# Kernel optimization log

Measured on AMD Instinct MI355X. Metric: run time of the kernel, lower is better.

## Reference

```python
import jax, jax.numpy as jnp
import numpy as np

DT = 0.01  # discretization step


def _discretize(log_omega, zeta_logit, P, Q, B):
    """Bilinear (Tustin) discretization of DPLR A = diag(lambda) + P Q^T."""
    omega = jnp.exp(log_omega)
    zeta = jax.nn.sigmoid(zeta_logit)
    real = -zeta * omega
    imag = omega * jnp.sqrt(jnp.clip(1.0 - zeta * zeta, 1e-8, None))
    lam = jax.lax.complex(real, imag)                      # (n,) complex eigenvalues
    A = jnp.diag(lam) + (P @ Q.T).astype(lam.dtype)        # (n, n) complex
    n = A.shape[0]
    I = jnp.eye(n, dtype=A.dtype)
    I_minus = I - (DT / 2.0) * A
    I_plus = I + (DT / 2.0) * A
    A_d = jnp.linalg.solve(I_minus, I_plus)                # (n, n)
    B_d = jnp.linalg.solve(I_minus, B.astype(A.dtype) * jnp.sqrt(jnp.float32(DT)))  # (n, d_in)
    return A_d, B_d


def setup_inputs() -> dict:
    key = jax.random.key(0)
    ks = jax.random.split(key, 8)
    n, r, d_in, d_out = 64, 4, 128, 128
    batch, seq = 32, 8192
    log_omega = jax.random.uniform(ks[0], (n,)) * (np.log(0.1) - np.log(0.01)) + np.log(0.01)
    return {
        "u": jax.random.normal(ks[1], (batch, seq, d_in), dtype=jnp.float32),
        "log_omega": log_omega.astype(jnp.float32),
        "zeta_logit": (jax.random.normal(ks[2], (n,)) * 0.5).astype(jnp.float32),
        "P": (jax.random.normal(ks[3], (n, r)) * 0.1).astype(jnp.float32),
        "Q": (jax.random.normal(ks[4], (n, r)) * 0.1).astype(jnp.float32),
        "B": (jax.random.normal(ks[5], (n, d_in)) * 0.1).astype(jnp.float32),
        "C": (jax.random.normal(ks[6], (d_out, n)) * 0.1).astype(jnp.float32),
        "D": jnp.zeros((d_out, d_in), dtype=jnp.float32),
    }


def reference(u, log_omega, zeta_logit, P, Q, B, C, D):
    A_d, B_d = _discretize(log_omega, zeta_logit, P, Q, B)
    cdt = A_d.dtype
    uc = u.astype(cdt)                                     # (b, t, d_in)
    # Precompute input injections and feedthrough as batched GEMMs.
    bu = jnp.einsum('bti,ni->btn', uc, B_d)                # (b, t, n)
    du = jnp.einsum('bti,oi->bto', uc, D.astype(cdt))      # (b, t, d_out)

    def step(x, bu_t):                                     # x: (b, n)
        x = x @ A_d.T + bu_t
        return x, x

    x0 = jnp.zeros((u.shape[0], A_d.shape[0]), dtype=cdt)
    _, xs = jax.lax.scan(step, x0, jnp.swapaxes(bu, 0, 1))  # (t, b, n)
    xs = jnp.swapaxes(xs, 0, 1)                             # (b, t, n)
    y = jnp.einsum('btn,on->bto', xs, C.astype(cdt)) + du
    return y.real
```

## Files before the change

### kernel.cpp

```cpp
#include <hip/hip_runtime.h>

#define OFF_E      0L
#define OFF_E2     8192L
#define OFF_AD     16384L
#define OFF_P0     24576L
#define OFF_P1     32768L
#define OFF_AHAT   40960L
#define OFF_ALHAT  57344L
#define OFF_WBU    73728L
#define OFF_EST    90112L
#define OFF_SIN    614400L
#define OFF_XR     1138688L
#define OFF_FW1H   8192L
#define OFF_FW1L   16384L
#define OFF_FCH    24576L
#define OFF_FCL    28672L
#define OFF_FDH    32768L
#define OFF_FDL    40960L

typedef __attribute__((ext_vector_type(8))) short short8;
typedef __attribute__((ext_vector_type(4))) float f32x4;

union U4S8 { uint4 u; short8 s; };
union S8U  { ushort h[8]; short8 s; };


__global__ void build_E(const float* __restrict__ lw, const float* __restrict__ zl,
                        const float* __restrict__ P, const float* __restrict__ Q,
                        float2* __restrict__ E)
{
    int idx = blockIdx.x * 256 + threadIdx.x;
    if (idx >= 4096) return;
    int i = idx >> 6, j = idx & 63;
    float pq = 0.f;
    #pragma unroll
    for (int r = 0; r < 4; ++r) pq += P[i*4+r] * Q[j*4+r];
    float ex = pq, ey = 0.f;
    if (i == j) {
        float om = expf(lw[i]);
        float ze = 1.f / (1.f + expf(-zl[i]));
        ex += -ze * om;
        ey  = om * sqrtf(fmaxf(1.f - ze*ze, 1e-8f));
    }
    E[idx] = make_float2(0.005f * ex, 0.005f * ey);
}

__global__ __launch_bounds__(256) void cgemm64(const float2* __restrict__ A,
                                               const float2* __restrict__ B,
                                               float2* __restrict__ Co,
                                               int aI, int bI, int post)
{
    int g = blockIdx.x * 256 + threadIdx.x;
    #pragma unroll
    for (int q = 0; q < 4; ++q) {
        int idx = g + q * 1024;
        int i = idx >> 6, j = idx & 63;
        float accx = 0.f, accy = 0.f;
        for (int k = 0; k < 64; ++k) {
            float2 a = A[i*64 + k];
            if (aI && k == i) a.x += 1.f;
            float2 b = B[k*64 + j];
            if (bI && k == j) b.x += 1.f;
            accx += a.x*b.x - a.y*b.y;
            accy += a.x*b.y + a.y*b.x;
        }
        if (post) { accx = 2.f*accx - (i == j ? 1.f : 0.f); accy = 2.f*accy; }
        Co[idx] = make_float2(accx, accy);
    }
}

__global__ __launch_bounds__(256) void k_bd(const float2* __restrict__ Ad,
                                            const float* __restrict__ Bm,
                                            float* __restrict__ Wbu)
{
    int idx = blockIdx.x * 256 + threadIdx.x;
    int n = idx >> 7, i = idx & 127;
    float ar = 0.f, ai = 0.f;
    for (int m = 0; m < 64; ++m) {
        float2 a = Ad[n*64 + m];
        float b = Bm[m*128 + i];
        ar += a.x * b; ai += a.y * b;
    }
    ar += Bm[n*128 + i];
    Wbu[n*128 + i]      = 0.05f * ar;
    Wbu[(64+n)*128 + i] = 0.05f * ai;
}

__global__ void k_embed(const float2* __restrict__ Ad, const float2* __restrict__ M64,
                        float* __restrict__ Ahat, float* __restrict__ ALhat)
{
    int idx = blockIdx.x * 256 + threadIdx.x;
    int sel = idx >> 14;
    int rem = idx & 16383;
    int i = rem >> 7, j = rem & 127;
    const float2* S = sel ? M64 : Ad;
    float2 v = S[(i & 63)*64 + (j & 63)];
    float o = (i < 64) ? ((j < 64) ? v.x : -v.y)
                       : ((j < 64) ? v.y :  v.x);
    (sel ? ALhat : Ahat)[i*128 + j] = o;
}

__global__ void k_swz(const float* __restrict__ Ahat, ushort* __restrict__ DTf)
{
    int t = blockIdx.x * 256 + threadIdx.x;
    if (t >= 2048) return;
    int lane = t & 63, kt = (t >> 6) & 3, nt = t >> 8;
    int n = (lane & 15) + nt * 16;
    int kbase = (lane >> 4) * 8 + kt * 32;
    #pragma unroll
    for (int j = 0; j < 8; ++j) {
        int k = kbase + j;
        float d = Ahat[n * 128 + k] - (n == k ? 1.f : 0.f);
        uint u = __float_as_uint(d);
        DTf[t * 8 + j] = (ushort)((u + 0x7FFFu + ((u >> 16) & 1)) >> 16);
    }
}

__device__ __forceinline__ ushort rne_bf16(float v) {
    uint u = __float_as_uint(v);
    return (ushort)((u + 0x7FFFu + ((u >> 16) & 1u)) >> 16);
}

__global__ void k_wfrag(const float* __restrict__ W, int KT,
                        ushort* __restrict__ FHi, ushort* __restrict__ FLo)
{
    int total = 8 * KT * 64;
    int t = blockIdx.x * 256 + threadIdx.x;
    if (t >= total) return;
    int K = KT * 32;
    int lane = t & 63;
    int kt = (t >> 6) % KT;
    int nt = t / (64 * KT);
    int n = (lane & 15) + nt * 16;
    int kbase = (lane >> 4) * 8 + kt * 32;
    #pragma unroll
    for (int j = 0; j < 8; ++j) {
        float v = W[n * K + kbase + j];
        ushort h = rne_bf16(v);
        float vh = __uint_as_float(((uint)h) << 16);
        ushort lo = rne_bf16(v - vh);
        FHi[t * 8 + j] = h;
        FLo[t * 8 + j] = lo;
    }
}

__device__ __forceinline__ void split8(const float* __restrict__ xf, short8& hi, short8& lo) {
    S8U H, L;
    #pragma unroll
    for (int j = 0; j < 8; ++j) {
        float v = xf[j];
        uint u = __float_as_uint(v);
        uint hbits = (u + 0x7FFFu + ((u >> 16) & 1u)) & 0xFFFF0000u;
        H.h[j] = (ushort)(hbits >> 16);
        float r = v - __uint_as_float(hbits);
        uint ur = __float_as_uint(r);
        L.h[j] = (ushort)((ur + 0x7FFFu + ((ur >> 16) & 1u)) >> 16);
    }
    hi = H.s; lo = L.s;
}

template<int KT1, int KT2>
__global__ __launch_bounds__(256) void gemm_mfma(
    const float* __restrict__ X1, const uint4* __restrict__ F1h, const uint4* __restrict__ F1l,
    const float* __restrict__ X2, const uint4* __restrict__ F2h, const uint4* __restrict__ F2l,
    float* __restrict__ Y)
{
    constexpr int KT2P = (KT2 > 0) ? KT2 : 1;
    int l = threadIdx.x & 63, w = threadIdx.x >> 6;
    int m = l & 15, q = l >> 4;

    short8 f1h[2][KT1], f1l[2][KT1];
    #pragma unroll
    for (int nt = 0; nt < 2; ++nt)
        #pragma unroll
        for (int kt = 0; kt < KT1; ++kt) {
            int f = ((w*2 + nt)*KT1 + kt)*64 + l;
            U4S8 a; a.u = F1h[f]; f1h[nt][kt] = a.s;
            U4S8 b; b.u = F1l[f]; f1l[nt][kt] = b.s;
        }
    short8 f2h[2][KT2P], f2l[2][KT2P];
    if constexpr (KT2 > 0) {
        #pragma unroll
        for (int nt = 0; nt < 2; ++nt)
            #pragma unroll
            for (int kt = 0; kt < KT2; ++kt) {
                int f = ((w*2 + nt)*KT2 + kt)*64 + l;
                U4S8 a; a.u = F2h[f]; f2h[nt][kt] = a.s;
                U4S8 b; b.u = F2l[f]; f2l[nt][kt] = b.s;
            }
    }

    long row0 = (long)blockIdx.x * 64;
    const float* x1p = X1 + (row0 + m) * (KT1*32) + q*8;
    const float* x2p = (KT2 > 0) ? (X2 + (row0 + m) * (KT2P*32) + q*8) : nullptr;
    float* yp = Y + (row0 + q*4) * 128 + w*32 + m;

    float4 xa[KT1 + KT2P][2], xb[KT1 + KT2P][2];

    auto loadt = [&](float4 (&dst)[KT1 + KT2P][2], int rt) {
        long o1 = (long)rt * 16 * (KT1*32);
        #pragma unroll
        for (int kt = 0; kt < KT1; ++kt) {
            const float* p = x1p + o1 + kt*32;
            dst[kt][0] = *(const float4*)p;
            dst[kt][1] = *(const float4*)(p + 4);
        }
        if constexpr (KT2 > 0) {
            long o2 = (long)rt * 16 * (KT2*32);
            #pragma unroll
            for (int kt = 0; kt < KT2; ++kt) {
                const float* p = x2p + o2 + kt*32;
                dst[KT1 + kt][0] = *(const float4*)p;
                dst[KT1 + kt][1] = *(const float4*)(p + 4);
            }
        }
    };

    auto compute = [&](float4 (&xr)[KT1 + KT2P][2], int rt) {
        f32x4 acc[2];
        acc[0] = (f32x4){0.f, 0.f, 0.f, 0.f};
        acc[1] = (f32x4){0.f, 0.f, 0.f, 0.f};
        #pragma unroll
        for (int kt = 0; kt < KT1; ++kt) {
            short8 ah, al;
            split8((const float*)&xr[kt][0], ah, al);
            #pragma unroll
            for (int nt = 0; nt < 2; ++nt) {
                acc[nt] = __builtin_amdgcn_mfma_f32_16x16x32_bf16(ah, f1h[nt][kt], acc[nt], 0, 0, 0);
                acc[nt] = __builtin_amdgcn_mfma_f32_16x16x32_bf16(al, f1h[nt][kt], acc[nt], 0, 0, 0);
                acc[nt] = __builtin_amdgcn_mfma_f32_16x16x32_bf16(ah, f1l[nt][kt], acc[nt], 0, 0, 0);
            }
        }
        if constexpr (KT2 > 0) {
            #pragma unroll
            for (int kt = 0; kt < KT2; ++kt) {
                short8 ah, al;
                split8((const float*)&xr[KT1 + kt][0], ah, al);
                #pragma unroll
                for (int nt = 0; nt < 2; ++nt) {
                    acc[nt] = __builtin_amdgcn_mfma_f32_16x16x32_bf16(ah, f2h[nt][kt], acc[nt], 0, 0, 0);
                    acc[nt] = __builtin_amdgcn_mfma_f32_16x16x32_bf16(al, f2h[nt][kt], acc[nt], 0, 0, 0);
                    acc[nt] = __builtin_amdgcn_mfma_f32_16x16x32_bf16(ah, f2l[nt][kt], acc[nt], 0, 0, 0);
                }
            }
        }
        #pragma unroll
        for (int nt = 0; nt < 2; ++nt)
            #pragma unroll
            for (int r = 0; r < 4; ++r)
                yp[(long)rt*16*128 + r*128 + nt*16] = acc[nt][r];
    };

    loadt(xa, 0);
    loadt(xb, 1);
    compute(xa, 0);
    loadt(xa, 2);
    compute(xb, 1);
    loadt(xb, 3);
    compute(xa, 2);
    compute(xb, 3);
}

template <int PASS>
__global__ __launch_bounds__(64, 1) void mfma_scan(
    const uint4* __restrict__ DTf, const float* __restrict__ bu,
    const float* __restrict__ sIn, float* __restrict__ eOut,
    float* __restrict__ xrOut)
{
    __shared__ ushort xlds[16 * 136];
    int l    = threadIdx.x;
    int col  = l & 15;
    int quad = l >> 4;
    int wid  = blockIdx.x;

    short8 dtf[8][4];
    #pragma unroll
    for (int nt = 0; nt < 8; ++nt)
        #pragma unroll
        for (int kt = 0; kt < 4; ++kt) {
            U4S8 u; u.u = DTf[(nt*4 + kt)*64 + l];
            dtf[nt][kt] = u.s;
        }

    int  rowg0 = wid * 16;
    long b  = rowg0 >> 7;
    long c0 = rowg0 & 127;

    f32x4 acc[8];
    #pragma unroll
    for (int nt = 0; nt < 8; ++nt) acc[nt] = (f32x4){0.f, 0.f, 0.f, 0.f};
    if constexpr (PASS == 3) {
        #pragma unroll
        for (int nt = 0; nt < 8; ++nt)
            #pragma unroll
            for (int r = 0; r < 4; ++r)
                acc[nt][r] = sIn[(long)(rowg0 + quad*4 + r)*128 + col + nt*16];
    }

    long buBase[4], xrBase[4];
    #pragma unroll
    for (int r = 0; r < 4; ++r) {
        int m = quad*4 + r;
        long tbase = b*8192 + (c0 + m)*64;
        buBase[r] = tbase*128 + col;
        xrBase[r] = tbase*64 + col;
    }

    float buA[8][4], buB[8][4];
    #define LOADBU(dst, TAU) { long _t = (TAU); _Pragma("unroll") \
        for (int nt = 0; nt < 8; ++nt) { _Pragma("unroll") \
            for (int r = 0; r < 4; ++r) dst[nt][r] = bu[buBase[r] + _t*128 + nt*16]; } }

    auto dostep = [&](float (&bucur)[8][4], int TAU) {
        asm volatile("" ::: "memory");
        #pragma unroll
        for (int nt = 0; nt < 8; ++nt)
            #pragma unroll
            for (int r = 0; r < 4; ++r) {
                uint u = __float_as_uint(acc[nt][r]);
                xlds[(quad*4 + r)*136 + col + nt*16] = (ushort)((u + 0x8000u) >> 16);
            }
        asm volatile("" ::: "memory");
        short8 af[4];
        #pragma unroll
        for (int kt = 0; kt < 4; ++kt) {
            U4S8 u; u.u = *(const uint4*)&xlds[col*136 + quad*8 + kt*32];
            af[kt] = u.s;
        }
        #pragma unroll
        for (int nt = 0; nt < 8; ++nt)
            #pragma unroll
            for (int r = 0; r < 4; ++r) acc[nt][r] += bucur[nt][r];
        #pragma unroll
        for (int kt = 0; kt < 4; ++kt)
            #pragma unroll
            for (int nt = 0; nt < 8; ++nt)
                acc[nt] = __builtin_amdgcn_mfma_f32_16x16x32_bf16(af[kt], dtf[nt][kt], acc[nt], 0, 0, 0);
        if constexpr (PASS == 3) {
            #pragma unroll
            for (int nt = 0; nt < 4; ++nt)
                #pragma unroll
                for (int r = 0; r < 4; ++r)
                    xrOut[xrBase[r] + (long)TAU*64 + nt*16] = acc[nt][r];
        }
    };

    LOADBU(buA, 0);
    for (int tau = 0; tau < 64; tau += 2) {
        LOADBU(buB, tau + 1);
        dostep(buA, tau);
        LOADBU(buA, (tau + 2 < 64) ? (tau + 2) : 63);
        dostep(buB, tau + 1);
    }

    if constexpr (PASS == 1) {
        #pragma unroll
        for (int nt = 0; nt < 8; ++nt)
            #pragma unroll
            for (int r = 0; r < 4; ++r)
                eOut[(long)(rowg0 + quad*4 + r)*128 + col + nt*16] = acc[nt][r];
    }
    #undef LOADBU
}

template <int PH>
__global__ __launch_bounds__(64, 1) void phase2k(
    const uint4* __restrict__ Bh, const uint4* __restrict__ Bl,
    const float* __restrict__ eIn, const float* __restrict__ seedIn,
    float* __restrict__ outPtr)
{
    constexpr int NSTEP = (PH == 2) ? 8 : 16;
    __shared__ ushort xh[16 * 136];
    __shared__ ushort xl[16 * 136];
    int l = threadIdx.x;
    int col = l & 15, quad = l >> 4;
    int wid = blockIdx.x;

    short8 bh[8][4], bl[8][4];
    #pragma unroll
    for (int nt = 0; nt < 8; ++nt)
        #pragma unroll
        for (int kt = 0; kt < 4; ++kt) {
            U4S8 a; a.u = Bh[(nt*4 + kt)*64 + l]; bh[nt][kt] = a.s;
            U4S8 b; b.u = Bl[(nt*4 + kt)*64 + l]; bl[nt][kt] = b.s;
        }

    long eBase[4], oBase[4];
    #pragma unroll
    for (int r = 0; r < 4; ++r) {
        int g = wid*16 + quad*4 + r;
        if constexpr (PH == 2) {
            eBase[r] = (long)g * 1024;
            oBase[r] = (long)g * 1024;
        } else {
            int b = g >> 3, seg = g & 7;
            eBase[r] = ((long)b*128 + seg*16) * 128;
            oBase[r] = (PH == 1) ? (long)g * 128 : eBase[r];
        }
    }

    f32x4 acc[8];
    #pragma unroll
    for (int nt = 0; nt < 8; ++nt) acc[nt] = (f32x4){0.f, 0.f, 0.f, 0.f};
    if constexpr (PH == 3) {
        #pragma unroll
        for (int nt = 0; nt < 8; ++nt)
            #pragma unroll
            for (int r = 0; r < 4; ++r)
                acc[nt][r] = seedIn[(long)(wid*16 + quad*4 + r)*128 + col + nt*16];
    }

    float eA[8][4], eB[8][4];
    #define LOADE(dst, C) { long _c = (C); _Pragma("unroll") \
        for (int nt = 0; nt < 8; ++nt) { _Pragma("unroll") \
            for (int r = 0; r < 4; ++r) dst[nt][r] = eIn[eBase[r] + _c*128 + col + nt*16]; } }

    auto dostep = [&](float (&ecur)[8][4], int c) {
        if constexpr (PH >= 2) {
            #pragma unroll
            for (int nt = 0; nt < 8; ++nt)
                #pragma unroll
                for (int r = 0; r < 4; ++r)
                    outPtr[oBase[r] + (long)c*128 + col + nt*16] = acc[nt][r];
        }
        asm volatile("" ::: "memory");
        #pragma unroll
        for (int nt = 0; nt < 8; ++nt)
            #pragma unroll
            for (int r = 0; r < 4; ++r) {
                float v = acc[nt][r];
                uint u = __float_as_uint(v);
                int off = (quad*4 + r)*136 + col + nt*16;
                xh[off] = (ushort)(u >> 16);
                float rr = v - __uint_as_float(u & 0xFFFF0000u);
                xl[off] = (ushort)(__float_as_uint(rr) >> 16);
            }
        asm volatile("" ::: "memory");
        short8 ah[4], al[4];
        #pragma unroll
        for (int kt = 0; kt < 4; ++kt) {
            U4S8 u1; u1.u = *(const uint4*)&xh[col*136 + quad*8 + kt*32]; ah[kt] = u1.s;
            U4S8 u2; u2.u = *(const uint4*)&xl[col*136 + quad*8 + kt*32]; al[kt] = u2.s;
        }
        #pragma unroll
        for (int nt = 0; nt < 8; ++nt)
            #pragma unroll
            for (int r = 0; r < 4; ++r) acc[nt][r] = ecur[nt][r];
        #pragma unroll
        for (int kt = 0; kt < 4; ++kt)
            #pragma unroll
            for (int nt = 0; nt < 8; ++nt)
                acc[nt] = __builtin_amdgcn_mfma_f32_16x16x32_bf16(ah[kt], bh[nt][kt], acc[nt], 0, 0, 0);
        #pragma unroll
        for (int kt = 0; kt < 4; ++kt)
            #pragma unroll
            for (int nt = 0; nt < 8; ++nt)
                acc[nt] = __builtin_amdgcn_mfma_f32_16x16x32_bf16(al[kt], bh[nt][kt], acc[nt], 0, 0, 0);
        #pragma unroll
        for (int kt = 0; kt < 4; ++kt)
            #pragma unroll
            for (int nt = 0; nt < 8; ++nt)
                acc[nt] = __builtin_amdgcn_mfma_f32_16x16x32_bf16(ah[kt], bl[nt][kt], acc[nt], 0, 0, 0);
    };

    LOADE(eA, 0);
    for (int c = 0; c < NSTEP; c += 2) {
        LOADE(eB, c + 1);
        dostep(eA, c);
        LOADE(eA, (c + 2 < NSTEP) ? (c + 2) : (NSTEP - 1));
        dostep(eB, c + 1);
    }

    if constexpr (PH == 1) {
        #pragma unroll
        for (int nt = 0; nt < 8; ++nt)
            #pragma unroll
            for (int r = 0; r < 4; ++r)
                outPtr[oBase[r] + col + nt*16] = acc[nt][r];
    }
    #undef LOADE
}


extern "C" void kernel_launch(void* const* d_in, const int* in_sizes, int n_in,
                              void* d_out, int out_size, void* d_ws, size_t ws_size,
                              hipStream_t stream) {
    const float* u  = (const float*)d_in[0];
    const float* lw = (const float*)d_in[1];
    const float* zl = (const float*)d_in[2];
    const float* P  = (const float*)d_in[3];
    const float* Q  = (const float*)d_in[4];
    const float* Bm = (const float*)d_in[5];
    const float* Cm = (const float*)d_in[6];
    const float* Dm = (const float*)d_in[7];
    float* y = (float*)d_out;
    float* w = (float*)d_ws;

    float2* E   = (float2*)(w + OFF_E);
    float2* E2  = (float2*)(w + OFF_E2);
    float2* AD  = (float2*)(w + OFF_AD);
    float2* P0  = (float2*)(w + OFF_P0);
    float2* P1  = (float2*)(w + OFF_P1);
    float*  Ahat  = w + OFF_AHAT;
    float*  ALhat = w + OFF_ALHAT;
    float*  Wbu   = w + OFF_WBU;
    float*  Est   = w + OFF_EST;
    float*  SIn   = w + OFF_SIN;
    float*  XR    = w + OFF_XR;
    ushort* DTf   = (ushort*)(w + OFF_E);
    ushort* FW1H  = (ushort*)(w + OFF_FW1H);
    ushort* FW1L  = (ushort*)(w + OFF_FW1L);
    ushort* FCH   = (ushort*)(w + OFF_FCH);
    ushort* FCL   = (ushort*)(w + OFF_FCL);
    ushort* FDH   = (ushort*)(w + OFF_FDH);
    ushort* FDL   = (ushort*)(w + OFF_FDL);
    float*  E2s   = w + OFF_XR;
    float*  S2s   = w + OFF_XR + 32768L;
    ushort* ALHH  = (ushort*)(w + OFF_XR + 65536L);
    ushort* ALHL  = (ushort*)(w + OFF_XR + 73728L);
    ushort* M16H  = (ushort*)(w + OFF_XR + 81920L);
    ushort* M16L  = (ushort*)(w + OFF_XR + 90112L);

    build_E<<<16, 256, 0, stream>>>(lw, zl, P, Q, E);
    cgemm64<<<4, 256, 0, stream>>>(E, E, E2, 0, 0, 0);
    cgemm64<<<4, 256, 0, stream>>>(E, E2, AD, 1, 1, 1);
    k_bd<<<32, 256, 0, stream>>>(AD, Bm, Wbu);
    cgemm64<<<4, 256, 0, stream>>>(AD, AD, P0, 0, 0, 0);
    cgemm64<<<4, 256, 0, stream>>>(P0, P0, P1, 0, 0, 0);
    cgemm64<<<4, 256, 0, stream>>>(P1, P1, P0, 0, 0, 0);
    cgemm64<<<4, 256, 0, stream>>>(P0, P0, P1, 0, 0, 0);
    cgemm64<<<4, 256, 0, stream>>>(P1, P1, P0, 0, 0, 0);
    cgemm64<<<4, 256, 0, stream>>>(P0, P0, P1, 0, 0, 0);
    k_embed<<<128, 256, 0, stream>>>(AD, P1, Ahat, ALhat);
    k_swz<<<8, 256, 0, stream>>>(Ahat, DTf);
    k_wfrag<<<8, 256, 0, stream>>>(ALhat, 4, ALHH, ALHL);
    cgemm64<<<4, 256, 0, stream>>>(P1, P1, P0, 0, 0, 0);
    cgemm64<<<4, 256, 0, stream>>>(P0, P0, P1, 0, 0, 0);
    cgemm64<<<4, 256, 0, stream>>>(P1, P1, P0, 0, 0, 0);
    cgemm64<<<4, 256, 0, stream>>>(P0, P0, P1, 0, 0, 0);
    k_embed<<<128, 256, 0, stream>>>(AD, P1, Ahat, ALhat);
    k_wfrag<<<8, 256, 0, stream>>>(ALhat, 4, M16H, M16L);
    k_wfrag<<<8, 256, 0, stream>>>(Wbu, 4, FW1H, FW1L);
    k_wfrag<<<4, 256, 0, stream>>>(Cm, 2, FCH, FCL);
    k_wfrag<<<8, 256, 0, stream>>>(Dm, 4, FDH, FDL);

    gemm_mfma<4, 0><<<4096, 256, 0, stream>>>(u, (const uint4*)FW1H, (const uint4*)FW1L,
                                              nullptr, nullptr, nullptr, y);

    mfma_scan<1><<<256, 64, 0, stream>>>((const uint4*)DTf, y, nullptr, Est, nullptr);
    phase2k<1><<<16, 64, 0, stream>>>((const uint4*)ALHH, (const uint4*)ALHL, Est, nullptr, E2s);
    phase2k<2><<<2, 64, 0, stream>>>((const uint4*)M16H, (const uint4*)M16L, E2s, nullptr, S2s);
    phase2k<3><<<16, 64, 0, stream>>>((const uint4*)ALHH, (const uint4*)ALHL, Est, S2s, SIn);
    mfma_scan<3><<<256, 64, 0, stream>>>((const uint4*)DTf, y, SIn, nullptr, XR);

    gemm_mfma<2, 4><<<4096, 256, 0, stream>>>(XR, (const uint4*)FCH, (const uint4*)FCL,
                                              u, (const uint4*)FDH, (const uint4*)FDL, y);
}
```

Measured before the change: 792.0 us.

## Store intermediates in bf16 and stage GEMM inputs through LDS with single-bf16 activations

The bu injection buffer and the scan's state output are now stored as bf16 instead of fp32, which halves the intermediate memory traffic between the GEMM and scan stages. The GEMM kernels stage activation tiles in LDS as bf16 and drop the hi/lo split of activations, cutting MFMA count from three to two per k-tile and removing the per-element split arithmetic. The cost is lower accuracy, since activations and intermediates keep only bf16 precision, plus an added LDS barrier that replaces the previous register double-buffered loads.

```diff
diff --git a/kernel.cpp b/kernel.cpp
--- a/kernel.cpp
+++ b/kernel.cpp
@@ -22,7 +22,6 @@
 typedef __attribute__((ext_vector_type(4))) float f32x4;
 
 union U4S8 { uint4 u; short8 s; };
-union S8U  { ushort h[8]; short8 s; };
 
 
 __global__ void build_E(const float* __restrict__ lw, const float* __restrict__ zl,
@@ -120,6 +119,9 @@
     uint u = __float_as_uint(v);
     return (ushort)((u + 0x7FFFu + ((u >> 16) & 1u)) >> 16);
 }
+__device__ __forceinline__ float bf2f(ushort h) {
+    return __uint_as_float(((uint)h) << 16);
+}
 
 __global__ void k_wfrag(const float* __restrict__ W, int KT,
                         ushort* __restrict__ FHi, ushort* __restrict__ FLo)
@@ -137,37 +139,61 @@
     for (int j = 0; j < 8; ++j) {
         float v = W[n * K + kbase + j];
         ushort h = rne_bf16(v);
-        float vh = __uint_as_float(((uint)h) << 16);
+        float vh = bf2f(h);
         ushort lo = rne_bf16(v - vh);
         FHi[t * 8 + j] = h;
         FLo[t * 8 + j] = lo;
     }
 }
 
-__device__ __forceinline__ void split8(const float* __restrict__ xf, short8& hi, short8& lo) {
-    S8U H, L;
-    #pragma unroll
-    for (int j = 0; j < 8; ++j) {
-        float v = xf[j];
-        uint u = __float_as_uint(v);
-        uint hbits = (u + 0x7FFFu + ((u >> 16) & 1u)) & 0xFFFF0000u;
-        H.h[j] = (ushort)(hbits >> 16);
-        float r = v - __uint_as_float(hbits);
-        uint ur = __float_as_uint(r);
-        L.h[j] = (ushort)((ur + 0x7FFFu + ((ur >> 16) & 1u)) >> 16);
-    }
-    hi = H.s; lo = L.s;
-}
-
-template<int KT1, int KT2>
-__global__ __launch_bounds__(256) void gemm_mfma(
-    const float* __restrict__ X1, const uint4* __restrict__ F1h, const uint4* __restrict__ F1l,
+template<int KT1, int KT2, int X1BF, int OUTBF>
+__global__ __launch_bounds__(256) void gemm_stage(
+    const void* __restrict__ X1v, const uint4* __restrict__ F1h, const uint4* __restrict__ F1l,
     const float* __restrict__ X2, const uint4* __restrict__ F2h, const uint4* __restrict__ F2l,
-    float* __restrict__ Y)
-{
+    void* __restrict__ Yv)
+{
+    constexpr int K1 = KT1 * 32;
+    constexpr int S1 = K1 + 8;
     constexpr int KT2P = (KT2 > 0) ? KT2 : 1;
-    int l = threadIdx.x & 63, w = threadIdx.x >> 6;
+    __shared__ ushort lds1[64 * S1];
+    __shared__ ushort lds2[(KT2 > 0) ? 64 * 136 : 8];
+
+    int t = threadIdx.x;
+    int l = t & 63, w = t >> 6;
     int m = l & 15, q = l >> 4;
+    long row0 = (long)blockIdx.x * 64;
+
+    if constexpr (X1BF == 0) {
+        const float* X1 = (const float*)X1v;
+        #pragma unroll
+        for (int rr = 0; rr < K1/16; ++rr) {
+            int idx = rr * 256 + t;
+            int row = idx / (K1/4), cq = idx % (K1/4);
+            float4 v = *(const float4*)&X1[(row0 + row) * K1 + cq*4];
+            ushort4 h;
+            h.x = rne_bf16(v.x); h.y = rne_bf16(v.y); h.z = rne_bf16(v.z); h.w = rne_bf16(v.w);
+            *(ushort4*)&lds1[row * S1 + cq*4] = h;
+        }
+    } else {
+        const ushort* X1 = (const ushort*)X1v;
+        #pragma unroll
+        for (int rr = 0; rr < K1/16; ++rr) {
+            int idx = rr * 256 + t;
+            int row = idx / (K1/4), cq = idx % (K1/4);
+            *(ushort4*)&lds1[row * S1 + cq*4] = *(const ushort4*)&X1[(row0 + row) * K1 + cq*4];
+        }
+    }
+    if constexpr (KT2 > 0) {
+        #pragma unroll
+        for (int rr = 0; rr < 8; ++rr) {
+            int idx = rr * 256 + t;
+            int row = idx >> 5, cq = idx & 31;
+            float4 v = *(const float4*)&X2[(row0 + row) * 128 + cq*4];
+            ushort4 h;
+            h.x = rne_bf16(v.x); h.y = rne_bf16(v.y); h.z = rne_bf16(v.z); h.w = rne_bf16(v.w);
+            *(ushort4*)&lds2[row * 136 + cq*4] = h;
+        }
+    }
 
     short8 f1h[2][KT1], f1l[2][KT1];
     #pragma unroll
@@ -190,82 +216,51 @@
             }
     }
 
-    long row0 = (long)blockIdx.x * 64;
-    const float* x1p = X1 + (row0 + m) * (KT1*32) + q*8;
-    const float* x2p = (KT2 > 0) ? (X2 + (row0 + m) * (KT2P*32) + q*8) : nullptr;
-    float* yp = Y + (row0 + q*4) * 128 + w*32 + m;
-
-    float4 xa[KT1 + KT2P][2], xb[KT1 + KT2P][2];
-
-    auto loadt = [&](float4 (&dst)[KT1 + KT2P][2], int rt) {
-        long o1 = (long)rt * 16 * (KT1*32);
-        #pragma unroll
-        for (int kt = 0; kt < KT1; ++kt) {
-            const float* p = x1p + o1 + kt*32;
-            dst[kt][0] = *(const float4*)p;
-            dst[kt][1] = *(const float4*)(p + 4);
-        }
-        if constexpr (KT2 > 0) {
-            long o2 = (long)rt * 16 * (KT2*32);
-            #pragma unroll
-            for (int kt = 0; kt < KT2; ++kt) {
-                const float* p = x2p + o2 + kt*32;
-                dst[KT1 + kt][0] = *(const float4*)p;
-                dst[KT1 + kt][1] = *(const float4*)(p + 4);
-            }
-        }
-    };
-
-    auto compute = [&](float4 (&xr)[KT1 + KT2P][2], int rt) {
+    __syncthreads();
+
+    float*  Yf = (float*)Yv;
+    ushort* Yb = (ushort*)Yv;
+    #pragma unroll
+    for (int rt = 0; rt < 4; ++rt) {
         f32x4 acc[2];
         acc[0] = (f32x4){0.f, 0.f, 0.f, 0.f};
         acc[1] = (f32x4){0.f, 0.f, 0.f, 0.f};
         #pragma unroll
         for (int kt = 0; kt < KT1; ++kt) {
-            short8 ah, al;
-            split8((const float*)&xr[kt][0], ah, al);
+            U4S8 a; a.u = *(const uint4*)&lds1[(rt*16 + m) * S1 + q*8 + kt*32];
             #pragma unroll
             for (int nt = 0; nt < 2; ++nt) {
-                acc[nt] = __builtin_amdgcn_mfma_f32_16x16x32_bf16(ah, f1h[nt][kt], acc[nt], 0, 0, 0);
-                acc[nt] = __builtin_amdgcn_mfma_f32_16x16x32_bf16(al, f1h[nt][kt], acc[nt], 0, 0, 0);
-                acc[nt] = __builtin_amdgcn_mfma_f32_16x16x32_bf16(ah, f1l[nt][kt], acc[nt], 0, 0, 0);
+                acc[nt] = __builtin_amdgcn_mfma_f32_16x16x32_bf16(a.s, f1h[nt][kt], acc[nt], 0, 0, 0);
+                acc[nt] = __builtin_amdgcn_mfma_f32_16x16x32_bf16(a.s, f1l[nt][kt], acc[nt], 0, 0, 0);
             }
         }
         if constexpr (KT2 > 0) {
             #pragma unroll
             for (int kt = 0; kt < KT2; ++kt) {
-                short8 ah, al;
-                split8((const float*)&xr[KT1 + kt][0], ah, al);
+                U4S8 a; a.u = *(const uint4*)&lds2[(rt*16 + m) * 136 + q*8 + kt*32];
                 #pragma unroll
                 for (int nt = 0; nt < 2; ++nt) {
-                    acc[nt] = __builtin_amdgcn_mfma_f32_16x16x32_bf16(ah, f2h[nt][kt], acc[nt], 0, 0, 0);
-                    acc[nt] = __builtin_amdgcn_mfma_f32_16x16x32_bf16(al, f2h[nt][kt], acc[nt], 0, 0, 0);
-                    acc[nt] = __builtin_amdgcn_mfma_f32_16x16x32_bf16(ah, f2l[nt][kt], acc[nt], 0, 0, 0);
+                    acc[nt] = __builtin_amdgcn_mfma_f32_16x16x32_bf16(a.s, f2h[nt][kt], acc[nt], 0, 0, 0);
+                    acc[nt] = __builtin_amdgcn_mfma_f32_16x16x32_bf16(a.s, f2l[nt][kt], acc[nt], 0, 0, 0);
                 }
             }
         }
         #pragma unroll
         for (int nt = 0; nt < 2; ++nt)
             #pragma unroll
-            for (int r = 0; r < 4; ++r)
-                yp[(long)rt*16*128 + r*128 + nt*16] = acc[nt][r];
-    };
-
-    loadt(xa, 0);
-    loadt(xb, 1);
-    compute(xa, 0);
-    loadt(xa, 2);
-    compute(xb, 1);
-    loadt(xb, 3);
-    compute(xa, 2);
-    compute(xb, 3);
+            for (int r = 0; r < 4; ++r) {
+                long o = (row0 + rt*16 + q*4 + r) * 128 + w*32 + nt*16 + m;
+                if constexpr (OUTBF) Yb[o] = rne_bf16(acc[nt][r]);
+                else                 Yf[o] = acc[nt][r];
+            }
+    }
 }
 
 template <int PASS>
 __global__ __launch_bounds__(64, 1) void mfma_scan(
-    const uint4* __restrict__ DTf, const float* __restrict__ bu,
+    const uint4* __restrict__ DTf, const ushort* __restrict__ bu,
     const float* __restrict__ sIn, float* __restrict__ eOut,
-    float* __restrict__ xrOut)
+    ushort* __restrict__ xrOut)
 {
     __shared__ ushort xlds[16 * 136];
     int l    = threadIdx.x;
@@ -309,7 +304,7 @@
     float buA[8][4], buB[8][4];
     #define LOADBU(dst, TAU) { long _t = (TAU); _Pragma("unroll") \
         for (int nt = 0; nt < 8; ++nt) { _Pragma("unroll") \
-            for (int r = 0; r < 4; ++r) dst[nt][r] = bu[buBase[r] + _t*128 + nt*16]; } }
+            for (int r = 0; r < 4; ++r) dst[nt][r] = bf2f(bu[buBase[r] + _t*128 + nt*16]); } }
 
     auto dostep = [&](float (&bucur)[8][4], int TAU) {
         asm volatile("" ::: "memory");
@@ -341,7 +336,7 @@
             for (int nt = 0; nt < 4; ++nt)
                 #pragma unroll
                 for (int r = 0; r < 4; ++r)
-                    xrOut[xrBase[r] + (long)TAU*64 + nt*16] = acc[nt][r];
+                    xrOut[xrBase[r] + (long)TAU*64 + nt*16] = rne_bf16(acc[nt][r]);
         }
     };
 
@@ -506,7 +501,7 @@
     float*  Wbu   = w + OFF_WBU;
     float*  Est   = w + OFF_EST;
     float*  SIn   = w + OFF_SIN;
-    float*  XR    = w + OFF_XR;
+    ushort* XRb   = (ushort*)(w + OFF_XR);
     ushort* DTf   = (ushort*)(w + OFF_E);
     ushort* FW1H  = (ushort*)(w + OFF_FW1H);
     ushort* FW1L  = (ushort*)(w + OFF_FW1L);
@@ -544,15 +539,17 @@
     k_wfrag<<<4, 256, 0, stream>>>(Cm, 2, FCH, FCL);
     k_wfrag<<<8, 256, 0, stream>>>(Dm, 4, FDH, FDL);
 
-    gemm_mfma<4, 0><<<4096, 256, 0, stream>>>(u, (const uint4*)FW1H, (const uint4*)FW1L,
-                                              nullptr, nullptr, nullptr, y);
-
-    mfma_scan<1><<<256, 64, 0, stream>>>((const uint4*)DTf, y, nullptr, Est, nullptr);
+    gemm_stage<4, 0, 0, 1><<<4096, 256, 0, stream>>>(
+        u, (const uint4*)FW1H, (const uint4*)FW1L,
+        nullptr, nullptr, nullptr, y);
+
+    mfma_scan<1><<<256, 64, 0, stream>>>((const uint4*)DTf, (const ushort*)y, nullptr, Est, nullptr);
     phase2k<1><<<16, 64, 0, stream>>>((const uint4*)ALHH, (const uint4*)ALHL, Est, nullptr, E2s);
     phase2k<2><<<2, 64, 0, stream>>>((const uint4*)M16H, (const uint4*)M16L, E2s, nullptr, S2s);
     phase2k<3><<<16, 64, 0, stream>>>((const uint4*)ALHH, (const uint4*)ALHL, Est, S2s, SIn);
-    mfma_scan<3><<<256, 64, 0, stream>>>((const uint4*)DTf, y, SIn, nullptr, XR);
-
-    gemm_mfma<2, 4><<<4096, 256, 0, stream>>>(XR, (const uint4*)FCH, (const uint4*)FCL,
-                                              u, (const uint4*)FDH, (const uint4*)FDL, y);
-}
+    mfma_scan<3><<<256, 64, 0, stream>>>((const uint4*)DTf, (const ushort*)y, SIn, nullptr, XRb);
+
+    gemm_stage<2, 4, 1, 0><<<4096, 256, 0, stream>>>(
+        XRb, (const uint4*)FCH, (const uint4*)FCL,
+        u, (const uint4*)FDH, (const uint4*)FDL, y);
+}
```

Result: faster. 689.2 us (-13.0%).
